# Optimization experiments

Measured on AMD Instinct MI355X. Metric: run time of the kernel, lower is better.

The kernel has to match this reference:

```python
import jax, jax.numpy as jnp
import numpy as np

TAU = 1.0
SCALE = 0.5
LN_EPS = 1e-5
NORM_EPS = 1e-12


def setup_inputs() -> dict:
    key = jax.random.key(0)
    k1, = jax.random.split(key, 1)
    N, D = 16384, 128
    x = jax.random.normal(k1, (N, D), dtype=jnp.float32)
    gamma = jnp.ones((D,), dtype=jnp.float32)
    beta = jnp.zeros((D,), dtype=jnp.float32)
    return {"x": x, "gamma": gamma, "beta": beta}


def reference(x, gamma, beta):
    # 'cn' branch: row-normalize, full pairwise cosine sim, row softmax, aggregate
    norm = jnp.sqrt(jnp.sum(x * x, axis=1, keepdims=True))
    norm_x = x / jnp.maximum(norm, NORM_EPS)          # [N, D]
    sim = jax.nn.softmax(norm_x @ norm_x.T / TAU, axis=1)  # [N, N]
    x_neg = sim @ x                                    # [N, D]
    y = (1.0 + SCALE) * x - SCALE * x_neg
    # LayerNorm over the hidden dim
    mu = jnp.mean(y, axis=-1, keepdims=True)
    var = jnp.mean((y - mu) ** 2, axis=-1, keepdims=True)
    return (y - mu) * jax.lax.rsqrt(var + LN_EPS) * gamma + beta
```

## Files before the change

### kernel.cpp

```cpp
#include <hip/hip_runtime.h>
#include <stdint.h>

#define NN 16384
#define DD 128
#define KT 64
#define QB 128

typedef float f32x16 __attribute__((ext_vector_type(16)));
typedef long long i64;

using gv = __attribute__((address_space(1))) const void;
using lv = __attribute__((address_space(3))) void;

__global__ void k_norm(const float* __restrict__ x, uint8_t* __restrict__ nx) {
  const int wave = threadIdx.x >> 6, lane = threadIdx.x & 63;
  const int row = blockIdx.x * 4 + wave;
  const float2 v = *reinterpret_cast<const float2*>(x + (size_t)row * DD + 2 * lane);
  float ss = v.x * v.x + v.y * v.y;
#pragma unroll
  for (int m = 1; m < 64; m <<= 1) ss += __shfl_xor(ss, m);
  const float rn = 1.2011224087f / fmaxf(sqrtf(ss), 1e-12f);
  const int w = __builtin_amdgcn_cvt_pk_fp8_f32(v.x * rn, v.y * rn, 0, false);
  *reinterpret_cast<uint16_t*>(nx + (size_t)row * DD + 2 * lane) = (uint16_t)w;
}

__global__ void k_transpose(const float* __restrict__ x, uint8_t* __restrict__ xT) {
  __shared__ uint16_t tile[64 * 66];
  const int n0 = blockIdx.x * 64;
  const int t = threadIdx.x;
#pragma unroll
  for (int e = 0; e < 16; ++e) {
    const int idx = e * 256 + t;
    const int r = idx >> 6, c2 = idx & 63;
    const float2 v = *reinterpret_cast<const float2*>(x + (size_t)(n0 + r) * DD + 2 * c2);
    const int w = __builtin_amdgcn_cvt_pk_fp8_f32(v.x, v.y, 0, false);
    tile[r * 66 + c2] = (uint16_t)w;
  }
  __syncthreads();
  const uint8_t* t8 = reinterpret_cast<const uint8_t*>(tile);
#pragma unroll
  for (int e = 0; e < 8; ++e) {
    const int idx = e * 256 + t;
    const int d = idx >> 4, n4 = (idx & 15) << 2;
    uint32_t w = (uint32_t)t8[(n4 + 0) * 132 + d];
    w |= (uint32_t)t8[(n4 + 1) * 132 + d] << 8;
    w |= (uint32_t)t8[(n4 + 2) * 132 + d] << 16;
    w |= (uint32_t)t8[(n4 + 3) * 132 + d] << 24;
    *reinterpret_cast<uint32_t*>(xT + (size_t)d * NN + n0 + n4) = w;
  }
}

__global__ __launch_bounds__(256, 3) void k_attn(
    const uint8_t* __restrict__ nx, const uint8_t* __restrict__ xT,
    float* __restrict__ Op, float* __restrict__ Lp, int nsplit) {
  __shared__ alignas(16) uint8_t Kb[3][KT * DD];
  __shared__ alignas(16) uint8_t Vb[3][DD * KT];

  const int tid = threadIdx.x;
  const int wave = tid >> 6;
  const int lane = tid & 63;
  const int rl = lane & 31;
  const int hi = lane >> 5;
  const int swzk = (rl & 7) << 4;
  const int swzv = ((rl >> 1) & 3) << 4;

  const int id = blockIdx.x;
  const int gs = 8 / nsplit;
  const int split = (id & 7) / gs;
  const int qblock = (id >> 3) * gs + (id & (gs - 1));

  const int nt = (NN / KT) / nsplit;
  const int t0s = split * nt;
  const int qw = qblock * QB + wave * 32;

  i64 q8[8];
#pragma unroll
  for (int dc = 0; dc < 8; ++dc)
    q8[dc] = *reinterpret_cast<const i64*>(nx + (size_t)(qw + rl) * DD + dc * 16 + 8 * hi);

  f32x16 o[4];
#pragma unroll
  for (int dt = 0; dt < 4; ++dt)
#pragma unroll
    for (int r = 0; r < 16; ++r) o[dt][r] = 0.f;
  float lsum = 0.f;

  auto stage = [&](int tt, int buf) {
    const int k0 = tt * KT;
#pragma unroll
    for (int jj = 0; jj < 2; ++jj) {
      const int j = wave * 2 + jj;
      const int A = j * 1024 + lane * 16;
      {
        const int row = A >> 7, b = A & 127;
        const uint8_t* src = nx + (size_t)(k0 + row) * DD + (b ^ ((row & 7) << 4));
        __builtin_amdgcn_global_load_lds((gv*)src,
            (lv*)(&Kb[buf][0] + j * 1024), 16, 0, 0);
      }
      {
        const int d = A >> 6, b2 = A & 63;
        const uint8_t* src = xT + (size_t)d * NN + k0 + (b2 ^ (((d >> 1) & 3) << 4));
        __builtin_amdgcn_global_load_lds((gv*)src,
            (lv*)(&Vb[buf][0] + j * 1024), 16, 0, 0);
      }
    }
  };

  stage(t0s + 0, 0);
  stage(t0s + 1, 1);

  for (int t = 0; t < nt; ++t) {
    __builtin_amdgcn_sched_barrier(0);
    if (t + 1 < nt) asm volatile("s_waitcnt vmcnt(4)" ::: "memory");
    else            asm volatile("s_waitcnt vmcnt(0)" ::: "memory");
    __builtin_amdgcn_s_barrier();
    __builtin_amdgcn_sched_barrier(0);
    if (t + 2 < nt) stage(t0s + t + 2, (t + 2) % 3);

    const int buf = t % 3;
    const uint8_t* kb = &Kb[buf][0];
    const uint8_t* vb = &Vb[buf][0];

    f32x16 s0, s1;
#pragma unroll
    for (int r = 0; r < 16; ++r) { s0[r] = 0.f; s1[r] = 0.f; }
    __builtin_amdgcn_s_setprio(1);
#pragma unroll
    for (int dc = 0; dc < 8; ++dc) {
      const int byt = (dc * 16 + 8 * hi) ^ swzk;
      const i64 ka0 = __builtin_bit_cast(i64, *reinterpret_cast<const uint2*>(kb + rl * 128 + byt));
      const i64 ka1 = __builtin_bit_cast(i64, *reinterpret_cast<const uint2*>(kb + 4096 + rl * 128 + byt));
      s0 = __builtin_amdgcn_mfma_f32_32x32x16_fp8_fp8(ka0, q8[dc], s0, 0, 0, 0);
      s1 = __builtin_amdgcn_mfma_f32_32x32x16_fp8_fp8(ka1, q8[dc], s1, 0, 0, 0);
    }
    __builtin_amdgcn_s_setprio(0);

    i64 pa[4];
#pragma unroll
    for (int kt = 0; kt < 2; ++kt) {
      float pe[16];
#pragma unroll
      for (int r = 0; r < 16; ++r) {
        const float sv = (kt == 0) ? s0[r] : s1[r];
        float p;
        asm("v_exp_f32 %0, %1" : "=v"(p) : "v"(sv));
        pe[r] = p;
        lsum += p;
      }
#pragma unroll
      for (int kc = 0; kc < 2; ++kc) {
        uint32_t wlo = (uint32_t)__builtin_amdgcn_cvt_pk_fp8_f32(pe[8 * kc + 0], pe[8 * kc + 1], 0, false);
        wlo = (uint32_t)__builtin_amdgcn_cvt_pk_fp8_f32(pe[8 * kc + 2], pe[8 * kc + 3], (int)wlo, true);
        uint32_t whi = (uint32_t)__builtin_amdgcn_cvt_pk_fp8_f32(pe[8 * kc + 4], pe[8 * kc + 5], 0, false);
        whi = (uint32_t)__builtin_amdgcn_cvt_pk_fp8_f32(pe[8 * kc + 6], pe[8 * kc + 7], (int)whi, true);
        asm("v_permlane32_swap_b32 %0, %1" : "+v"(wlo), "+v"(whi));
        const uint2 pd = {wlo, whi};
        pa[kt * 2 + kc] = __builtin_bit_cast(i64, pd);
      }
    }

    __builtin_amdgcn_s_setprio(1);
#pragma unroll
    for (int c4 = 0; c4 < 4; ++c4) {
      const int cb = (c4 * 16 + 8 * hi) ^ swzv;
#pragma unroll
      for (int dt = 0; dt < 4; ++dt) {
        const i64 vf = __builtin_bit_cast(i64,
            *reinterpret_cast<const uint2*>(vb + (dt * 32 + rl) * 64 + cb));
        o[dt] = __builtin_amdgcn_mfma_f32_32x32x16_fp8_fp8(pa[c4], vf, o[dt], 0, 0, 0);
      }
    }
    __builtin_amdgcn_s_setprio(0);
  }

  const float lt = lsum + __shfl_xor(lsum, 32);
  if (hi == 0) Lp[(size_t)split * NN + qw + rl] = lt;

  float* Ob = Op + (size_t)split * NN * DD;
#pragma unroll
  for (int dt = 0; dt < 4; ++dt)
#pragma unroll
    for (int r = 0; r < 16; ++r) {
      const int q = (r & 3) + 8 * (r >> 2) + 4 * hi;
      Ob[(size_t)(qw + q) * DD + dt * 32 + rl] = o[dt][r];
    }
}

__global__ void k_final(const float* __restrict__ x, const float* __restrict__ gamma,
                        const float* __restrict__ beta, const float* __restrict__ Op,
                        const float* __restrict__ Lp, float* __restrict__ out, int nsplit) {
  const int wave = threadIdx.x >> 6, lane = threadIdx.x & 63;
  const int row = blockIdx.x * 4 + wave;
  float o0 = 0.f, o1 = 0.f, lt = 0.f;
  for (int s = 0; s < nsplit; ++s) {
    const float2 v = *reinterpret_cast<const float2*>(
        Op + (size_t)s * NN * DD + (size_t)row * DD + 2 * lane);
    o0 += v.x;
    o1 += v.y;
    lt += Lp[(size_t)s * NN + row];
  }
  const float inv = 1.0f / lt;
  const float2 xv = *reinterpret_cast<const float2*>(x + (size_t)row * DD + 2 * lane);
  float y0 = 1.5f * xv.x - 0.5f * o0 * inv;
  float y1 = 1.5f * xv.y - 0.5f * o1 * inv;
  float sum = y0 + y1;
#pragma unroll
  for (int m = 1; m < 64; m <<= 1) sum += __shfl_xor(sum, m);
  const float mu = sum * (1.0f / 128.0f);
  const float d0 = y0 - mu, d1 = y1 - mu;
  float vs = d0 * d0 + d1 * d1;
#pragma unroll
  for (int m = 1; m < 64; m <<= 1) vs += __shfl_xor(vs, m);
  const float rs = rsqrtf(vs * (1.0f / 128.0f) + 1e-5f);
  const float2 g = *reinterpret_cast<const float2*>(gamma + 2 * lane);
  const float2 b = *reinterpret_cast<const float2*>(beta + 2 * lane);
  float2 ov;
  ov.x = d0 * rs * g.x + b.x;
  ov.y = d1 * rs * g.y + b.y;
  *reinterpret_cast<float2*>(out + (size_t)row * DD + 2 * lane) = ov;
}

extern "C" void kernel_launch(void* const* d_in, const int* in_sizes, int n_in,
                              void* d_out, int out_size, void* d_ws, size_t ws_size,
                              hipStream_t stream) {
  const float* x = (const float*)d_in[0];
  const float* gamma = (const float*)d_in[1];
  const float* beta = (const float*)d_in[2];
  float* out = (float*)d_out;
  char* ws = (char*)d_ws;

  uint8_t* nx = (uint8_t*)ws;
  uint8_t* xT = (uint8_t*)(ws + (size_t)NN * DD);
  const size_t base = (size_t)2 * NN * DD;
  const size_t per = (size_t)NN * DD * 4 + (size_t)NN * 4;

  int nsplit = 1;
  if (ws_size >= base + 4 * per) nsplit = 4;
  else if (ws_size >= base + 2 * per) nsplit = 2;

  float* Op = (float*)(ws + base);
  float* Lp = (float*)(ws + base + (size_t)nsplit * NN * DD * 4);

  k_norm<<<NN / 4, 256, 0, stream>>>(x, nx);
  k_transpose<<<NN / 64, 256, 0, stream>>>(x, xT);
  k_attn<<<dim3((NN / QB) * nsplit), 256, 0, stream>>>(nx, xT, Op, Lp, nsplit);
  k_final<<<NN / 4, 256, 0, stream>>>(x, gamma, beta, Op, Lp, out, nsplit);
}
```

Measured before the change: 133.1 us.

## Switch attention kernel to padded double-buffered LDS with split-wave staging and 8-way split

Replaces the XOR-swizzled triple-buffered K/V LDS tiles with padded-stride (144/72-byte) double buffers, so bank conflicts are avoided by padding instead of swizzle. Half the waves now stage K and the other half stage V, using precomputed offsets. Occupancy is raised to 4 blocks per CU. QK and softmax are interleaved per 32-key half, and the split count is templated with up to 8 key splits to add parallelism. The cost is shallower prefetch: each iteration waits for all loads, and more splits mean more partial-output traffic in the final reduction.

After: 135.6 us. Within noise of the previous version (+1.9%).

```diff
diff --git a/kernel.cpp b/kernel.cpp
--- a/kernel.cpp
+++ b/kernel.cpp
@@ -5,6 +5,10 @@
 #define DD 128
 #define KT 64
 #define QB 128
+#define KSTR 144
+#define VSTR 72
+#define KBYTES 9216
+#define VBYTES 9216
 
 typedef float f32x16 __attribute__((ext_vector_type(16)));
 typedef long long i64;
@@ -50,29 +54,56 @@
   }
 }
 
-__global__ __launch_bounds__(256, 3) void k_attn(
+template <int NSPLIT>
+__global__ __launch_bounds__(256, 4) void k_attn(
     const uint8_t* __restrict__ nx, const uint8_t* __restrict__ xT,
-    float* __restrict__ Op, float* __restrict__ Lp, int nsplit) {
-  __shared__ alignas(16) uint8_t Kb[3][KT * DD];
-  __shared__ alignas(16) uint8_t Vb[3][DD * KT];
+    float* __restrict__ Op, float* __restrict__ Lp) {
+  __shared__ alignas(16) uint8_t Kb[2][KBYTES];
+  __shared__ alignas(16) uint8_t Vb[2][VBYTES];
 
   const int tid = threadIdx.x;
   const int wave = tid >> 6;
   const int lane = tid & 63;
   const int rl = lane & 31;
   const int hi = lane >> 5;
-  const int swzk = (rl & 7) << 4;
-  const int swzv = ((rl >> 1) & 3) << 4;
 
   const int id = blockIdx.x;
-  const int gs = 8 / nsplit;
+  constexpr int gs = 8 / NSPLIT;
   const int split = (id & 7) / gs;
   const int qblock = (id >> 3) * gs + (id & (gs - 1));
 
-  const int nt = (NN / KT) / nsplit;
+  constexpr int nt = (NN / KT) / NSPLIT;
   const int t0s = split * nt;
   const int qw = qblock * QB + wave * 32;
 
+  const int sw = wave >> 1;
+  const int j0 = (wave & 1) * 5;
+  const int cnt = (wave & 1) ? 4 : 5;
+  uint32_t soff[5];
+#pragma unroll
+  for (int i = 0; i < 5; ++i) {
+    const int j = j0 + i;
+    const int t16 = j * 64 + lane;
+    if (sw == 0) {
+      soff[i] = (uint32_t)((t16 / 9) * DD + (t16 % 9) * 16);
+    } else {
+      const int d = (2 * t16) / 9;
+      const int c0 = t16 * 16 - d * VSTR;
+      soff[i] = (uint32_t)(d * NN + c0 + (c0 >= 64 ? (NN - VSTR) : 0));
+    }
+  }
+
+  auto stage = [&](int tt, int buf) {
+    const int k0 = tt * KT;
+    const uint8_t* basep = (sw == 0) ? (nx + (size_t)k0 * DD) : (xT + k0);
+    uint8_t* ldsb = (sw == 0) ? &Kb[buf][0] : &Vb[buf][0];
+#pragma unroll
+    for (int i = 0; i < 5; ++i)
+      if (i < cnt)
+        __builtin_amdgcn_global_load_lds((gv*)(basep + soff[i]),
+            (lv*)(ldsb + (j0 + i) * 1024), 16, 0, 0);
+  };
+
   i64 q8[8];
 #pragma unroll
   for (int dc = 0; dc < 8; ++dc)
@@ -85,74 +116,49 @@
     for (int r = 0; r < 16; ++r) o[dt][r] = 0.f;
   float lsum = 0.f;
 
-  auto stage = [&](int tt, int buf) {
-    const int k0 = tt * KT;
-#pragma unroll
-    for (int jj = 0; jj < 2; ++jj) {
-      const int j = wave * 2 + jj;
-      const int A = j * 1024 + lane * 16;
-      {
-        const int row = A >> 7, b = A & 127;
-        const uint8_t* src = nx + (size_t)(k0 + row) * DD + (b ^ ((row & 7) << 4));
-        __builtin_amdgcn_global_load_lds((gv*)src,
-            (lv*)(&Kb[buf][0] + j * 1024), 16, 0, 0);
-      }
-      {
-        const int d = A >> 6, b2 = A & 63;
-        const uint8_t* src = xT + (size_t)d * NN + k0 + (b2 ^ (((d >> 1) & 3) << 4));
-        __builtin_amdgcn_global_load_lds((gv*)src,
-            (lv*)(&Vb[buf][0] + j * 1024), 16, 0, 0);
-      }
-    }
-  };
-
-  stage(t0s + 0, 0);
-  stage(t0s + 1, 1);
+  stage(t0s, 0);
 
   for (int t = 0; t < nt; ++t) {
+    const int buf = t & 1;
     __builtin_amdgcn_sched_barrier(0);
-    if (t + 1 < nt) asm volatile("s_waitcnt vmcnt(4)" ::: "memory");
-    else            asm volatile("s_waitcnt vmcnt(0)" ::: "memory");
+    asm volatile("s_waitcnt vmcnt(0)" ::: "memory");
+    __builtin_amdgcn_sched_barrier(0);
     __builtin_amdgcn_s_barrier();
     __builtin_amdgcn_sched_barrier(0);
-    if (t + 2 < nt) stage(t0s + t + 2, (t + 2) % 3);
-
-    const int buf = t % 3;
+    if (t + 1 < nt) stage(t0s + t + 1, buf ^ 1);
+
     const uint8_t* kb = &Kb[buf][0];
     const uint8_t* vb = &Vb[buf][0];
-
-    f32x16 s0, s1;
-#pragma unroll
-    for (int r = 0; r < 16; ++r) { s0[r] = 0.f; s1[r] = 0.f; }
-    __builtin_amdgcn_s_setprio(1);
-#pragma unroll
-    for (int dc = 0; dc < 8; ++dc) {
-      const int byt = (dc * 16 + 8 * hi) ^ swzk;
-      const i64 ka0 = __builtin_bit_cast(i64, *reinterpret_cast<const uint2*>(kb + rl * 128 + byt));
-      const i64 ka1 = __builtin_bit_cast(i64, *reinterpret_cast<const uint2*>(kb + 4096 + rl * 128 + byt));
-      s0 = __builtin_amdgcn_mfma_f32_32x32x16_fp8_fp8(ka0, q8[dc], s0, 0, 0, 0);
-      s1 = __builtin_amdgcn_mfma_f32_32x32x16_fp8_fp8(ka1, q8[dc], s1, 0, 0, 0);
-    }
-    __builtin_amdgcn_s_setprio(0);
-
     i64 pa[4];
+
 #pragma unroll
     for (int kt = 0; kt < 2; ++kt) {
-      float pe[16];
-#pragma unroll
-      for (int r = 0; r < 16; ++r) {
-        const float sv = (kt == 0) ? s0[r] : s1[r];
-        float p;
-        asm("v_exp_f32 %0, %1" : "=v"(p) : "v"(sv));
-        pe[r] = p;
-        lsum += p;
+      const uint8_t* kbb = kb + kt * 32 * KSTR;
+      f32x16 s;
+#pragma unroll
+      for (int r = 0; r < 16; ++r) s[r] = 0.f;
+      __builtin_amdgcn_s_setprio(1);
+#pragma unroll
+      for (int dc = 0; dc < 8; ++dc) {
+        const i64 ka = __builtin_bit_cast(i64,
+            *reinterpret_cast<const uint2*>(kbb + rl * KSTR + dc * 16 + 8 * hi));
+        s = __builtin_amdgcn_mfma_f32_32x32x16_fp8_fp8(ka, q8[dc], s, 0, 0, 0);
       }
+      __builtin_amdgcn_s_setprio(0);
 #pragma unroll
       for (int kc = 0; kc < 2; ++kc) {
-        uint32_t wlo = (uint32_t)__builtin_amdgcn_cvt_pk_fp8_f32(pe[8 * kc + 0], pe[8 * kc + 1], 0, false);
-        wlo = (uint32_t)__builtin_amdgcn_cvt_pk_fp8_f32(pe[8 * kc + 2], pe[8 * kc + 3], (int)wlo, true);
-        uint32_t whi = (uint32_t)__builtin_amdgcn_cvt_pk_fp8_f32(pe[8 * kc + 4], pe[8 * kc + 5], 0, false);
-        whi = (uint32_t)__builtin_amdgcn_cvt_pk_fp8_f32(pe[8 * kc + 6], pe[8 * kc + 7], (int)whi, true);
+        float e[8];
+#pragma unroll
+        for (int j = 0; j < 8; ++j) {
+          float p;
+          asm("v_exp_f32 %0, %1" : "=v"(p) : "v"(s[8 * kc + j]));
+          e[j] = p;
+          lsum += p;
+        }
+        uint32_t wlo = (uint32_t)__builtin_amdgcn_cvt_pk_fp8_f32(e[0], e[1], 0, false);
+        wlo = (uint32_t)__builtin_amdgcn_cvt_pk_fp8_f32(e[2], e[3], (int)wlo, true);
+        uint32_t whi = (uint32_t)__builtin_amdgcn_cvt_pk_fp8_f32(e[4], e[5], 0, false);
+        whi = (uint32_t)__builtin_amdgcn_cvt_pk_fp8_f32(e[6], e[7], (int)whi, true);
         asm("v_permlane32_swap_b32 %0, %1" : "+v"(wlo), "+v"(whi));
         const uint2 pd = {wlo, whi};
         pa[kt * 2 + kc] = __builtin_bit_cast(i64, pd);
@@ -162,11 +168,11 @@
     __builtin_amdgcn_s_setprio(1);
 #pragma unroll
     for (int c4 = 0; c4 < 4; ++c4) {
-      const int cb = (c4 * 16 + 8 * hi) ^ swzv;
+      const int cb = c4 * 16 + 8 * hi;
 #pragma unroll
       for (int dt = 0; dt < 4; ++dt) {
         const i64 vf = __builtin_bit_cast(i64,
-            *reinterpret_cast<const uint2*>(vb + (dt * 32 + rl) * 64 + cb));
+            *reinterpret_cast<const uint2*>(vb + (dt * 32 + rl) * VSTR + cb));
         o[dt] = __builtin_amdgcn_mfma_f32_32x32x16_fp8_fp8(pa[c4], vf, o[dt], 0, 0, 0);
       }
     }
@@ -234,15 +240,20 @@
   const size_t base = (size_t)2 * NN * DD;
   const size_t per = (size_t)NN * DD * 4 + (size_t)NN * 4;
 
-  int nsplit = 1;
-  if (ws_size >= base + 4 * per) nsplit = 4;
-  else if (ws_size >= base + 2 * per) nsplit = 2;
+  int nsplit = 2;
+  if (ws_size >= base + 8 * per) nsplit = 8;
+  else if (ws_size >= base + 4 * per) nsplit = 4;
 
   float* Op = (float*)(ws + base);
   float* Lp = (float*)(ws + base + (size_t)nsplit * NN * DD * 4);
 
   k_norm<<<NN / 4, 256, 0, stream>>>(x, nx);
   k_transpose<<<NN / 64, 256, 0, stream>>>(x, xT);
-  k_attn<<<dim3((NN / QB) * nsplit), 256, 0, stream>>>(nx, xT, Op, Lp, nsplit);
+  if (nsplit == 8)
+    k_attn<8><<<dim3((NN / QB) * 8), 256, 0, stream>>>(nx, xT, Op, Lp);
+  else if (nsplit == 4)
+    k_attn<4><<<dim3((NN / QB) * 4), 256, 0, stream>>>(nx, xT, Op, Lp);
+  else
+    k_attn<2><<<dim3((NN / QB) * 2), 256, 0, stream>>>(nx, xT, Op, Lp);
   k_final<<<NN / 4, 256, 0, stream>>>(x, gamma, beta, Op, Lp, out, nsplit);
 }
```
